# Performance work log

Measured on AMD Instinct MI355X. Metric: run time of the kernel, lower is better.

Reference implementation:

```python
import jax, jax.numpy as jnp
import numpy as np

N = 20000        # number of protein atoms
C_IN = 32        # input atom features
C = 128          # hidden_channels
E_BOND = 80000   # directed bond edges (~2 bonds/atom, both directions)
R = 4.0          # radius_graph radius (Angstrom)
BOX = 55.0       # box side -> ~32 neighbors within r=4


def _radius_graph_np(pos, r):
    # symmetric radius graph, no self loops (PyG radius_graph, neighbor cap omitted)
    r2 = r * r
    rows, cols = [], []
    for i0 in range(0, pos.shape[0], 500):
        chunk = pos[i0:i0 + 500]
        d2 = ((chunk[:, None, :] - pos[None, :, :]) ** 2).sum(-1)
        m = d2 < r2
        m[np.arange(chunk.shape[0]), i0 + np.arange(chunk.shape[0])] = False
        ii, jj = np.nonzero(m)
        rows.append(jj)            # source j
        cols.append(ii + i0)       # target i
    return np.stack([np.concatenate(rows), np.concatenate(cols)]).astype(np.int32)


def setup_inputs() -> dict:
    key = jax.random.key(0)
    ks = jax.random.split(key, 12)
    rng = np.random.default_rng(0)

    pos = rng.uniform(0.0, BOX, (N, 3)).astype(np.float32)
    r_edge_index = jnp.asarray(_radius_graph_np(pos, R))

    half = E_BOND // 2
    s = rng.integers(0, N, half); d = rng.integers(0, N, half)
    edge_index = jnp.asarray(np.stack([np.concatenate([s, d]), np.concatenate([d, s])]).astype(np.int32))

    def lin(k, fin, fout):
        lim = 1.0 / np.sqrt(fin)
        kw, kb = jax.random.split(k)
        W = jax.random.uniform(kw, (fin, fout), jnp.float32, -lim, lim)
        b = jax.random.uniform(kb, (fout,), jnp.float32, -lim, lim)
        return W, b

    We1, be1 = lin(ks[0], C_IN, C)
    We2, be2 = lin(ks[1], C, C)
    Wf1, bf1 = lin(ks[2], 2 * C, C); Ws1, bs1 = lin(ks[3], 2 * C, C)
    Wf2, bf2 = lin(ks[4], 2 * C, C); Ws2, bs2 = lin(ks[5], 2 * C, C)
    Wf3, bf3 = lin(ks[6], 2 * C, C); Ws3, bs3 = lin(ks[7], 2 * C, C)
    Wf4, bf4 = lin(ks[8], 2 * C, C); Ws4, bs4 = lin(ks[9], 2 * C, C)

    x_prot = jax.random.normal(ks[10], (N, C_IN), jnp.float32)
    v_prot = jnp.asarray(pos)

    return dict(x_prot=x_prot, v_prot=v_prot, edge_index=edge_index, r_edge_index=r_edge_index,
                We1=We1, be1=be1, We2=We2, be2=be2,
                Wf1=Wf1, bf1=bf1, Ws1=Ws1, bs1=bs1,
                Wf2=Wf2, bf2=bf2, Ws2=Ws2, bs2=bs2,
                Wf3=Wf3, bf3=bf3, Ws3=Ws3, bs3=bs3,
                Wf4=Wf4, bf4=bf4, Ws4=Ws4, bs4=bs4)


def _cgconv(x, ei, Wf, bf, Ws, bs):
    # PyG CGConv: z = [x_i, x_j]; out = x + mean_j sigmoid(lin_f(z)) * softplus(lin_s(z))
    src, dst = ei[0], ei[1]              # source j -> target i
    z = jnp.concatenate([x[dst], x[src]], axis=1)          # [E, 2C]
    msg = jax.nn.sigmoid(z @ Wf + bf) * jax.nn.softplus(z @ Ws + bs)  # [E, C]
    agg = jax.ops.segment_sum(msg, dst, num_segments=x.shape[0])
    cnt = jax.ops.segment_sum(jnp.ones((ei.shape[1],), x.dtype), dst, num_segments=x.shape[0])
    return x + agg / jnp.maximum(cnt, 1.0)[:, None]


def reference(x_prot, v_prot, edge_index, r_edge_index,
              We1, be1, We2, be2,
              Wf1, bf1, Ws1, bs1, Wf2, bf2, Ws2, bs2,
              Wf3, bf3, Ws3, bs3, Wf4, bf4, Ws4, bs4):
    # embed MLP (PyG MLP with batch-norm at init == identity): Linear->ReLU->Linear
    x = jax.nn.relu(x_prot @ We1 + be1) @ We2 + be2
    # bond convs
    x = jax.nn.relu(_cgconv(x, edge_index, Wf1, bf1, Ws1, bs1))
    x = jax.nn.relu(_cgconv(x, edge_index, Wf2, bf2, Ws2, bs2))
    # radius convs (r_edge_index = radius_graph(v_prot, r=4), precomputed in setup)
    x = jax.nn.relu(_cgconv(x, r_edge_index, Wf3, bf3, Ws3, bs3))
    x = jax.nn.relu(_cgconv(x, r_edge_index, Wf4, bf4, Ws4, bs4))
    return jax.nn.relu(x)  # final self.act (idempotent on ReLU output)
```

## Files before the change

kernel.cpp:

```cpp
#include <hip/hip_runtime.h>
#include <hip/hip_bf16.h>

#define NN 20000
#define CC 128

typedef __attribute__((ext_vector_type(8))) _Float16 half8;
typedef __attribute__((ext_vector_type(2))) _Float16 half2v;
typedef __attribute__((ext_vector_type(4))) float f32x4;

typedef const __attribute__((address_space(1))) void gv_t;
typedef __attribute__((address_space(3))) void sv_t;

__global__ __launch_bounds__(256) void conv_all_kernel(
    const float* __restrict__ Wf0, const float* __restrict__ Ws0,
    const float* __restrict__ Wf1, const float* __restrict__ Ws1,
    const float* __restrict__ Wf2, const float* __restrict__ Ws2,
    const float* __restrict__ Wf3, const float* __restrict__ Ws3,
    const float* __restrict__ We2, const float* __restrict__ We1,
    const float* __restrict__ xprot,
    _Float16* __restrict__ WctAll, _Float16* __restrict__ Wcte,
    _Float16* __restrict__ Wt1, _Float16* __restrict__ xp16) {
    int id = blockIdx.x * 256 + threadIdx.x;
    if (id < 262144) {
        int Lw = id >> 16;
        int i = id & 65535;
        int c = i & 511;
        int k = i >> 9;
        const float* Wfp = (Lw == 0) ? Wf0 : (Lw == 1) ? Wf1 : (Lw == 2) ? Wf2 : Wf3;
        const float* Wsp = (Lw == 0) ? Ws0 : (Lw == 1) ? Ws1 : (Lw == 2) ? Ws2 : Ws3;
        float v;
        if (c < 128) v = Wfp[k * 128 + c];
        else if (c < 256) v = Wfp[(128 + k) * 128 + (c - 128)];
        else if (c < 384) v = Wsp[k * 128 + (c - 256)];
        else v = Wsp[(128 + k) * 128 + (c - 384)];
        WctAll[Lw * 65536 + c * 128 + k] = (_Float16)v;
    } else if (id < 278528) {
        int i = id - 262144;
        int c = i & 127;
        int k = i >> 7;
        Wcte[c * 128 + k] = (_Float16)We2[k * 128 + c];
    } else if (id < 282624) {
        int i = id - 278528;
        int c = i & 127;
        int k = i >> 7;
        Wt1[c * 32 + k] = (_Float16)We1[k * 128 + c];
    } else {
        int i = id - 282624;
        xp16[i] = (_Float16)xprot[i];
    }
}

__global__ __launch_bounds__(256) void enc1_mfma_kernel(
    const _Float16* __restrict__ A, const _Float16* __restrict__ Wt1,
    const float* __restrict__ b, _Float16* __restrict__ Y) {
    int t = threadIdx.x;
    int wid = t >> 6, l = t & 63;
    int lr = l & 15, hi = l >> 4;
    int m0 = blockIdx.x * 128 + wid * 32;
    half8 af[2];
#pragma unroll
    for (int m = 0; m < 2; ++m) {
        int row = m0 + m * 16 + lr;
        half8 v = {0, 0, 0, 0, 0, 0, 0, 0};
        if (row < NN) v = *(const half8*)(A + (long)row * 32 + hi * 8);
        af[m] = v;
    }
    f32x4 acc[2][8] = {};
#pragma unroll
    for (int n = 0; n < 8; ++n) {
        int col = n * 16 + lr;
        half8 bg = *(const half8*)(Wt1 + (long)col * 32 + hi * 8);
#pragma unroll
        for (int m = 0; m < 2; ++m)
            acc[m][n] = __builtin_amdgcn_mfma_f32_16x16x32_f16(af[m], bg, acc[m][n], 0, 0, 0);
    }
#pragma unroll
    for (int n = 0; n < 8; ++n) {
        int col = n * 16 + lr;
        float bb = b[col];
#pragma unroll
        for (int m = 0; m < 2; ++m) {
#pragma unroll
            for (int q = 0; q < 4; ++q) {
                int row = m0 + m * 16 + hi * 4 + q;
                if (row < NN)
                    Y[(long)row * 128 + col] = (_Float16)fmaxf(acc[m][n][q] + bb, 0.0f);
            }
        }
    }
}

__global__ __launch_bounds__(256) void gemm_mfma_kernel(
    const _Float16* __restrict__ A, const _Float16* __restrict__ Wt,
    const float* __restrict__ bias0, const float* __restrict__ bias1,
    _Float16* __restrict__ outH, float* __restrict__ outF,
    _Float16* __restrict__ outF16, int M, int mode) {
    __shared__ _Float16 lds[32768];
    int t = threadIdx.x;
    int w = t >> 6, l = t & 63;
    int m0 = blockIdx.x * 128;
    int n0 = blockIdx.y * 128;
    {
        int rin = l >> 4;
        int cs = l & 15;
#pragma unroll
        for (int j = 0; j < 8; ++j) {
            int r = w * 32 + j * 4 + rin;
            int g = cs ^ (r & 7);
            int grow = m0 + r;
            if (grow > M - 1) grow = M - 1;
            const _Float16* srcA = A + (long)grow * 128 + g * 8;
            __builtin_amdgcn_global_load_lds((gv_t*)srcA,
                (sv_t*)&lds[(w * 32 + j * 4) * 128], 16, 0, 0);
            const _Float16* srcB = Wt + (long)(n0 + r) * 128 + g * 8;
            __builtin_amdgcn_global_load_lds((gv_t*)srcB,
                (sv_t*)&lds[16384 + (w * 32 + j * 4) * 128], 16, 0, 0);
        }
    }
    __syncthreads();
    int wm = w >> 1, wn = w & 1;
    int lr = l & 15, hi = l >> 4;
    f32x4 acc[4][4] = {};
#pragma unroll
    for (int ks = 0; ks < 4; ++ks) {
        int cidx = 4 * ks + hi;
        half8 af[4], bg[4];
#pragma unroll
        for (int m = 0; m < 4; ++m) {
            int row = wm * 64 + m * 16 + lr;
            af[m] = *(const half8*)(&lds[row * 128 + (cidx ^ (row & 7)) * 8]);
        }
#pragma unroll
        for (int n = 0; n < 4; ++n) {
            int row = wn * 64 + n * 16 + lr;
            bg[n] = *(const half8*)(&lds[16384 + row * 128 + (cidx ^ (row & 7)) * 8]);
        }
#pragma unroll
        for (int m = 0; m < 4; ++m)
#pragma unroll
            for (int n = 0; n < 4; ++n)
                acc[m][n] = __builtin_amdgcn_mfma_f32_16x16x32_f16(
                    af[m], bg[n], acc[m][n], 0, 0, 0);
    }
    if (mode == 0) {
        __syncthreads();
        const float S = 1.44269504f;
#pragma unroll
        for (int n = 0; n < 4; ++n) {
            int cl = wn * 64 + n * 16 + lr;
            int gcol = n0 + cl;
            float badd = (gcol < 128) ? bias0[gcol]
                       : ((gcol >= 256 && gcol < 384) ? bias1[gcol - 256] : 0.0f);
#pragma unroll
            for (int m = 0; m < 4; ++m)
#pragma unroll
                for (int q = 0; q < 4; ++q) {
                    int rl = wm * 64 + m * 16 + hi * 4 + q;
                    lds[rl * 144 + cl] = (_Float16)((acc[m][n][q] + badd) * S);
                }
        }
        __syncthreads();
#pragma unroll
        for (int i = 0; i < 8; ++i) {
            int id = t + 256 * i;
            int row = id >> 4, ch = id & 15;
            int grow = m0 + row;
            if (grow < M) {
                half8 v = *(const half8*)(&lds[row * 144 + ch * 8]);
                *(half8*)(&outH[(long)grow * 512 + n0 + ch * 8]) = v;
            }
        }
    } else {
#pragma unroll
        for (int n = 0; n < 4; ++n) {
            int gcol = n0 + wn * 64 + n * 16 + lr;
            float badd = bias0[gcol];
#pragma unroll
            for (int m = 0; m < 4; ++m)
#pragma unroll
                for (int q = 0; q < 4; ++q) {
                    int grow = m0 + wm * 64 + m * 16 + hi * 4 + q;
                    if (grow < M) {
                        float v = acc[m][n][q] + badd;
                        outF[(long)grow * 128 + gcol] = v;
                        outF16[(long)grow * 128 + gcol] = (_Float16)v;
                    }
                }
        }
    }
}

__global__ __launch_bounds__(256) void count_int_kernel(
    const int* __restrict__ dst, int E, int* __restrict__ cnt) {
    int e = blockIdx.x * 256 + threadIdx.x;
    if (e < E) atomicAdd(&cnt[dst[e]], 1);
}

__global__ __launch_bounds__(1024) void scan_kernel(
    const int* __restrict__ cnt, int* __restrict__ off) {
    __shared__ int part[1024];
    int t = threadIdx.x;
    int base = t * 20;
    int loc[20];
    int s = 0;
#pragma unroll
    for (int i = 0; i < 20; ++i) {
        int idx = base + i;
        int v = (idx < NN) ? cnt[idx] : 0;
        loc[i] = s;
        s += v;
    }
    part[t] = s;
    __syncthreads();
    for (int d = 1; d < 1024; d <<= 1) {
        int v = (t >= d) ? part[t - d] : 0;
        __syncthreads();
        part[t] += v;
        __syncthreads();
    }
    int pre = (t > 0) ? part[t - 1] : 0;
#pragma unroll
    for (int i = 0; i < 20; ++i) {
        int idx = base + i;
        if (idx < NN) off[idx] = pre + loc[i];
    }
    if (t == 1023) off[NN] = part[1023];
}

__global__ __launch_bounds__(256) void scatter_kernel(
    const int* __restrict__ src, const int* __restrict__ dst, int E,
    const int* __restrict__ off, int* __restrict__ cur, int* __restrict__ eid) {
    int e = blockIdx.x * 256 + threadIdx.x;
    if (e < E) {
        int d = dst[e];
        int p = off[d] + atomicAdd(&cur[d], 1);
        eid[p] = src[e];
    }
}

__global__ __launch_bounds__(256) void csr_off_kernel(
    const int* __restrict__ dst, int E, int N1, int* __restrict__ off) {
    int n = blockIdx.x * 256 + threadIdx.x;
    if (n >= N1) return;
    int lo = 0, hi = E;
    while (lo < hi) {
        int mid = (lo + hi) >> 1;
        if (dst[mid] < n) lo = mid + 1;
        else hi = mid;
    }
    off[n] = lo;
}

__global__ __launch_bounds__(256) void node_agg_kernel(
    const _Float16* __restrict__ H, const int* __restrict__ srcArr,
    const int* __restrict__ off, const float* __restrict__ xin,
    float* __restrict__ xout, _Float16* __restrict__ xh, int write_h) {
    int n = blockIdx.x * 4 + (threadIdx.x >> 6);
    int nu = __builtin_amdgcn_readfirstlane(n);
    int l = threadIdx.x & 63;
    const half2v* H2 = (const half2v*)H;
    const half2v* hrow = H2 + (long)nu * 256;
    half2v fdh = hrow[l];
    half2v sdh = hrow[128 + l];
    int e0 = __builtin_amdgcn_readfirstlane(off[nu]);
    int e1 = __builtin_amdgcn_readfirstlane(off[nu + 1]);
    float ax = 0.0f, ay = 0.0f;
#define EDGEC(fv, sv)                                                        \
    {                                                                        \
        half2v fsum = fdh + (fv);                                            \
        half2v ssum = sdh + (sv);                                            \
        float fx = (float)fsum.x, fy = (float)fsum.y;                        \
        float sx = (float)ssum.x, sy = (float)ssum.y;                        \
        float rx = __builtin_amdgcn_rcpf(1.0f + __builtin_amdgcn_exp2f(-fx)); \
        float ry = __builtin_amdgcn_rcpf(1.0f + __builtin_amdgcn_exp2f(-fy)); \
        float spx = fmaxf(sx, 0.0f) +                                        \
                    __builtin_amdgcn_logf(1.0f + __builtin_amdgcn_exp2f(-fabsf(sx))); \
        float spy = fmaxf(sy, 0.0f) +                                        \
                    __builtin_amdgcn_logf(1.0f + __builtin_amdgcn_exp2f(-fabsf(sy))); \
        ax += rx * spx;                                                      \
        ay += ry * spy;                                                      \
    }
    int e = e0;
    for (; e + 3 < e1; e += 4) {
        int s0 = srcArr[e], s1 = srcArr[e + 1];
        int s2 = srcArr[e + 2], s3 = srcArr[e + 3];
        const half2v* h0 = H2 + (long)s0 * 256;
        const half2v* h1 = H2 + (long)s1 * 256;
        const half2v* h2 = H2 + (long)s2 * 256;
        const half2v* h3 = H2 + (long)s3 * 256;
        half2v f0 = h0[64 + l], g0 = h0[192 + l];
        half2v f1 = h1[64 + l], g1 = h1[192 + l];
        half2v f2 = h2[64 + l], g2 = h2[192 + l];
        half2v f3 = h3[64 + l], g3 = h3[192 + l];
        EDGEC(f0, g0) EDGEC(f1, g1) EDGEC(f2, g2) EDGEC(f3, g3)
    }
    for (; e < e1; ++e) {
        int s0 = srcArr[e];
        const half2v* h0 = H2 + (long)s0 * 256;
        half2v f0 = h0[64 + l], g0 = h0[192 + l];
        EDGEC(f0, g0)
    }
#undef EDGEC
    float inv = 0.6931471805599453f *
                __builtin_amdgcn_rcpf(fmaxf((float)(e1 - e0), 1.0f));
    float2 xv = ((const float2*)xin)[(long)nu * 64 + l];
    float ox = fmaxf(xv.x + ax * inv, 0.0f);
    float oy = fmaxf(xv.y + ay * inv, 0.0f);
    ((float2*)xout)[(long)nu * 64 + l] = make_float2(ox, oy);
    if (write_h) {
        half2v oh;
        oh.x = (_Float16)ox;
        oh.y = (_Float16)oy;
        ((half2v*)xh)[(long)nu * 64 + l] = oh;
    }
}

extern "C" void kernel_launch(void* const* d_in, const int* in_sizes, int n_in,
                              void* d_out, int out_size, void* d_ws, size_t ws_size,
                              hipStream_t stream) {
    const float* x_prot = (const float*)d_in[0];
    const int* eb = (const int*)d_in[2];
    const int* er = (const int*)d_in[3];
    int Eb = in_sizes[2] / 2;
    int Er = in_sizes[3] / 2;
    const float* We1 = (const float*)d_in[4];
    const float* be1 = (const float*)d_in[5];
    const float* We2 = (const float*)d_in[6];
    const float* be2 = (const float*)d_in[7];
    const float* Wf[4]  = {(const float*)d_in[8],  (const float*)d_in[12],
                           (const float*)d_in[16], (const float*)d_in[20]};
    const float* bf[4]  = {(const float*)d_in[9],  (const float*)d_in[13],
                           (const float*)d_in[17], (const float*)d_in[21]};
    const float* Wsp[4] = {(const float*)d_in[10], (const float*)d_in[14],
                           (const float*)d_in[18], (const float*)d_in[22]};
    const float* bsp[4] = {(const float*)d_in[11], (const float*)d_in[15],
                           (const float*)d_in[19], (const float*)d_in[23]};

    char* ws = (char*)d_ws;
    float*     xbuf  = (float*)ws;
    _Float16*  xhf   = (_Float16*)(ws + 10240000);
    _Float16*  H     = (_Float16*)(ws + 15360000);
    _Float16*  xp16  = (_Float16*)(ws + 35840000);
    int*       cntI  = (int*)(ws + 37120000);
    int*       curB  = (int*)(ws + 37200000);
    int*       offB  = (int*)(ws + 37280000);
    int*       offR  = (int*)(ws + 37360016);
    int*       eidB  = (int*)(ws + 37440032);
    _Float16*  WctAll= (_Float16*)(ws + 37760032);
    _Float16*  Wcte  = (_Float16*)(ws + 38284320);
    _Float16*  Wt1   = (_Float16*)(ws + 38317088);

    const int* srcB = eb;
    const int* dstB = eb + Eb;
    const int* srcR = er;

    conv_all_kernel<<<3604, 256, 0, stream>>>(
        Wf[0], Wsp[0], Wf[1], Wsp[1], Wf[2], Wsp[2], Wf[3], Wsp[3],
        We2, We1, x_prot, WctAll, Wcte, Wt1, xp16);

    hipMemsetAsync(cntI, 0, 160000, stream);
    count_int_kernel<<<(Eb + 255) / 256, 256, 0, stream>>>(dstB, Eb, cntI);
    scan_kernel<<<1, 1024, 0, stream>>>(cntI, offB);
    scatter_kernel<<<(Eb + 255) / 256, 256, 0, stream>>>(srcB, dstB, Eb, offB, curB, eidB);
    csr_off_kernel<<<(NN + 256) / 256, 256, 0, stream>>>(er + Er, Er, NN + 1, offR);

    enc1_mfma_kernel<<<157, 256, 0, stream>>>(xp16, Wt1, be1, H);
    {
        dim3 g(157, 1);
        gemm_mfma_kernel<<<g, 256, 0, stream>>>(H, Wcte, be2, be2, nullptr,
                                                xbuf, xhf, NN, 1);
    }

    for (int L = 0; L < 4; ++L) {
        dim3 g(157, 4);
        gemm_mfma_kernel<<<g, 256, 0, stream>>>(xhf, WctAll + L * 65536, bf[L],
                                                bsp[L], H, nullptr, nullptr, NN, 0);
        const int* sArr = (L < 2) ? eidB : srcR;
        const int* oArr = (L < 2) ? offB : offR;
        float* xout = (L == 3) ? (float*)d_out : xbuf;
        node_agg_kernel<<<NN / 4, 256, 0, stream>>>(H, sArr, oArr, xbuf, xout,
                                                    xhf, (L == 3) ? 0 : 1);
    }
    (void)n_in; (void)out_size; (void)ws_size;
}
```

Before: 230.4 us.

## Replace sigmoid/softplus transcendentals with LDS lookup tables in node aggregation

Precomputes a 2048-entry sigmoid table and a 1024-entry softplus-correction table (in log2 domain) on the GPU, loads them into shared memory per block, and replaces per-edge exp/rcp/log calls with clamped table lookups. The aggregation kernel also becomes a grid-stride loop over nodes with 2048 blocks, which amortizes the table load across many nodes. This trades transcendental ALU work for LDS reads and adds quantization error from nearest-bin lookup over a clamped range.

Result: slower. 239.4 us (+3.9%).

```diff
diff --git a/kernel.cpp b/kernel.cpp
--- a/kernel.cpp
+++ b/kernel.cpp
@@ -10,6 +10,8 @@
 
 typedef const __attribute__((address_space(1))) void gv_t;
 typedef __attribute__((address_space(3))) void sv_t;
+
+#define TBL_SCALE 85.333336f
 
 __global__ __launch_bounds__(256) void conv_all_kernel(
     const float* __restrict__ Wf0, const float* __restrict__ Ws0,
@@ -19,7 +21,8 @@
     const float* __restrict__ We2, const float* __restrict__ We1,
     const float* __restrict__ xprot,
     _Float16* __restrict__ WctAll, _Float16* __restrict__ Wcte,
-    _Float16* __restrict__ Wt1, _Float16* __restrict__ xp16) {
+    _Float16* __restrict__ Wt1, _Float16* __restrict__ xp16,
+    float* __restrict__ tbl) {
     int id = blockIdx.x * 256 + threadIdx.x;
     if (id < 262144) {
         int Lw = id >> 16;
@@ -44,9 +47,17 @@
         int c = i & 127;
         int k = i >> 7;
         Wt1[c * 32 + k] = (_Float16)We1[k * 128 + c];
-    } else {
+    } else if (id < 922624) {
         int i = id - 282624;
         xp16[i] = (_Float16)xprot[i];
+    } else if (id < 924672) {
+        int i = id - 922624;
+        float fp = (i + 0.5f) * (24.0f / 2048.0f) - 12.0f;
+        tbl[i] = 1.0f / (1.0f + exp2f(-fp));
+    } else if (id < 925696) {
+        int j = id - 924672;
+        float tt = (j + 0.5f) * (12.0f / 1024.0f);
+        tbl[2048 + j] = log2f(1.0f + exp2f(-tt));
     }
 }
 
@@ -254,64 +265,78 @@
 __global__ __launch_bounds__(256) void node_agg_kernel(
     const _Float16* __restrict__ H, const int* __restrict__ srcArr,
     const int* __restrict__ off, const float* __restrict__ xin,
-    float* __restrict__ xout, _Float16* __restrict__ xh, int write_h) {
-    int n = blockIdx.x * 4 + (threadIdx.x >> 6);
-    int nu = __builtin_amdgcn_readfirstlane(n);
-    int l = threadIdx.x & 63;
+    float* __restrict__ xout, _Float16* __restrict__ xh,
+    const float* __restrict__ tblG, int write_h) {
+    __shared__ float sigT[2048];
+    __shared__ float cT[1024];
+    int t = threadIdx.x;
+    for (int i = t; i < 3072; i += 256) {
+        float v = tblG[i];
+        if (i < 2048) sigT[i] = v;
+        else cT[i - 2048] = v;
+    }
+    __syncthreads();
+    int l = t & 63;
+    int wn = t >> 6;
     const half2v* H2 = (const half2v*)H;
-    const half2v* hrow = H2 + (long)nu * 256;
-    half2v fdh = hrow[l];
-    half2v sdh = hrow[128 + l];
-    int e0 = __builtin_amdgcn_readfirstlane(off[nu]);
-    int e1 = __builtin_amdgcn_readfirstlane(off[nu + 1]);
-    float ax = 0.0f, ay = 0.0f;
-#define EDGEC(fv, sv)                                                        \
-    {                                                                        \
-        half2v fsum = fdh + (fv);                                            \
-        half2v ssum = sdh + (sv);                                            \
-        float fx = (float)fsum.x, fy = (float)fsum.y;                        \
-        float sx = (float)ssum.x, sy = (float)ssum.y;                        \
-        float rx = __builtin_amdgcn_rcpf(1.0f + __builtin_amdgcn_exp2f(-fx)); \
-        float ry = __builtin_amdgcn_rcpf(1.0f + __builtin_amdgcn_exp2f(-fy)); \
-        float spx = fmaxf(sx, 0.0f) +                                        \
-                    __builtin_amdgcn_logf(1.0f + __builtin_amdgcn_exp2f(-fabsf(sx))); \
-        float spy = fmaxf(sy, 0.0f) +                                        \
-                    __builtin_amdgcn_logf(1.0f + __builtin_amdgcn_exp2f(-fabsf(sy))); \
-        ax += rx * spx;                                                      \
-        ay += ry * spy;                                                      \
-    }
-    int e = e0;
-    for (; e + 3 < e1; e += 4) {
-        int s0 = srcArr[e], s1 = srcArr[e + 1];
-        int s2 = srcArr[e + 2], s3 = srcArr[e + 3];
-        const half2v* h0 = H2 + (long)s0 * 256;
-        const half2v* h1 = H2 + (long)s1 * 256;
-        const half2v* h2 = H2 + (long)s2 * 256;
-        const half2v* h3 = H2 + (long)s3 * 256;
-        half2v f0 = h0[64 + l], g0 = h0[192 + l];
-        half2v f1 = h1[64 + l], g1 = h1[192 + l];
-        half2v f2 = h2[64 + l], g2 = h2[192 + l];
-        half2v f3 = h3[64 + l], g3 = h3[192 + l];
-        EDGEC(f0, g0) EDGEC(f1, g1) EDGEC(f2, g2) EDGEC(f3, g3)
-    }
-    for (; e < e1; ++e) {
-        int s0 = srcArr[e];
-        const half2v* h0 = H2 + (long)s0 * 256;
-        half2v f0 = h0[64 + l], g0 = h0[192 + l];
-        EDGEC(f0, g0)
-    }
+    for (int n = blockIdx.x * 4 + wn; n < NN; n += gridDim.x * 4) {
+        int nu = __builtin_amdgcn_readfirstlane(n);
+        const half2v* hrow = H2 + (long)nu * 256;
+        half2v fdh = hrow[l];
+        half2v sdh = hrow[128 + l];
+        int e0 = __builtin_amdgcn_readfirstlane(off[nu]);
+        int e1 = __builtin_amdgcn_readfirstlane(off[nu + 1]);
+        float ax = 0.0f, ay = 0.0f;
+#define EDGEC(fv, sv)                                                      \
+    {                                                                      \
+        half2v fsum = fdh + (fv);                                          \
+        half2v ssum = sdh + (sv);                                          \
+        float fx = (float)fsum.x, fy = (float)fsum.y;                      \
+        float sx = (float)ssum.x, sy = (float)ssum.y;                      \
+        float tfx = fminf(fmaxf(__builtin_fmaf(fx, TBL_SCALE, 1024.0f), 0.0f), 2047.0f); \
+        float tfy = fminf(fmaxf(__builtin_fmaf(fy, TBL_SCALE, 1024.0f), 0.0f), 2047.0f); \
+        float tsx = fminf(fabsf(sx) * TBL_SCALE, 1023.0f);                 \
+        float tsy = fminf(fabsf(sy) * TBL_SCALE, 1023.0f);                 \
+        float gx = sigT[(int)tfx];                                         \
+        float gy = sigT[(int)tfy];                                         \
+        float spx = fmaxf(sx, 0.0f) + cT[(int)tsx];                        \
+        float spy = fmaxf(sy, 0.0f) + cT[(int)tsy];                        \
+        ax += gx * spx;                                                    \
+        ay += gy * spy;                                                    \
+    }
+        int e = e0;
+        for (; e + 3 < e1; e += 4) {
+            int s0 = srcArr[e], s1 = srcArr[e + 1];
+            int s2 = srcArr[e + 2], s3 = srcArr[e + 3];
+            const half2v* h0 = H2 + (long)s0 * 256;
+            const half2v* h1 = H2 + (long)s1 * 256;
+            const half2v* h2 = H2 + (long)s2 * 256;
+            const half2v* h3 = H2 + (long)s3 * 256;
+            half2v f0 = h0[64 + l], g0 = h0[192 + l];
+            half2v f1 = h1[64 + l], g1 = h1[192 + l];
+            half2v f2 = h2[64 + l], g2 = h2[192 + l];
+            half2v f3 = h3[64 + l], g3 = h3[192 + l];
+            EDGEC(f0, g0) EDGEC(f1, g1) EDGEC(f2, g2) EDGEC(f3, g3)
+        }
+        for (; e < e1; ++e) {
+            int s0 = srcArr[e];
+            const half2v* h0 = H2 + (long)s0 * 256;
+            half2v f0 = h0[64 + l], g0 = h0[192 + l];
+            EDGEC(f0, g0)
+        }
 #undef EDGEC
-    float inv = 0.6931471805599453f *
-                __builtin_amdgcn_rcpf(fmaxf((float)(e1 - e0), 1.0f));
-    float2 xv = ((const float2*)xin)[(long)nu * 64 + l];
-    float ox = fmaxf(xv.x + ax * inv, 0.0f);
-    float oy = fmaxf(xv.y + ay * inv, 0.0f);
-    ((float2*)xout)[(long)nu * 64 + l] = make_float2(ox, oy);
-    if (write_h) {
-        half2v oh;
-        oh.x = (_Float16)ox;
-        oh.y = (_Float16)oy;
-        ((half2v*)xh)[(long)nu * 64 + l] = oh;
+        float inv = 0.6931471805599453f *
+                    __builtin_amdgcn_rcpf(fmaxf((float)(e1 - e0), 1.0f));
+        float2 xv = ((const float2*)xin)[(long)nu * 64 + l];
+        float ox = fmaxf(xv.x + ax * inv, 0.0f);
+        float oy = fmaxf(xv.y + ay * inv, 0.0f);
+        ((float2*)xout)[(long)nu * 64 + l] = make_float2(ox, oy);
+        if (write_h) {
+            half2v oh;
+            oh.x = (_Float16)ox;
+            oh.y = (_Float16)oy;
+            ((half2v*)xh)[(long)nu * 64 + l] = oh;
+        }
     }
 }
 
@@ -349,14 +374,15 @@
     _Float16*  WctAll= (_Float16*)(ws + 37760032);
     _Float16*  Wcte  = (_Float16*)(ws + 38284320);
     _Float16*  Wt1   = (_Float16*)(ws + 38317088);
+    float*     tbl   = (float*)(ws + 38325280);
 
     const int* srcB = eb;
     const int* dstB = eb + Eb;
     const int* srcR = er;
 
-    conv_all_kernel<<<3604, 256, 0, stream>>>(
+    conv_all_kernel<<<3616, 256, 0, stream>>>(
         Wf[0], Wsp[0], Wf[1], Wsp[1], Wf[2], Wsp[2], Wf[3], Wsp[3],
-        We2, We1, x_prot, WctAll, Wcte, Wt1, xp16);
+        We2, We1, x_prot, WctAll, Wcte, Wt1, xp16, tbl);
 
     hipMemsetAsync(cntI, 0, 160000, stream);
     count_int_kernel<<<(Eb + 255) / 256, 256, 0, stream>>>(dstB, Eb, cntI);
@@ -378,8 +404,8 @@
         const int* sArr = (L < 2) ? eidB : srcR;
         const int* oArr = (L < 2) ? offB : offR;
         float* xout = (L == 3) ? (float*)d_out : xbuf;
-        node_agg_kernel<<<NN / 4, 256, 0, stream>>>(H, sArr, oArr, xbuf, xout,
-                                                    xhf, (L == 3) ? 0 : 1);
+        node_agg_kernel<<<2048, 256, 0, stream>>>(H, sArr, oArr, xbuf, xout,
+                                                  xhf, tbl, (L == 3) ? 0 : 1);
     }
     (void)n_in; (void)out_size; (void)ws_size;
 }
```

## Store source-side gate projections in FP8 and interleave per-node H layout

Applied to the files above, without the earlier changes.

The projection output H is repacked so each node's destination-side FP16 filter and softplus values sit interleaved, followed by FP8-quantized source-side values packed as filter/softplus pairs. The aggregation kernel then gathers only 4 bytes per lane per neighbor instead of two 4-byte FP16 loads from separate regions. This cuts gather traffic across the roughly 640K radius edges. In exchange, source-side precision drops to FP8, which risks accuracy, and the GEMM epilogue now issues narrower scattered stores.

After: 258.7 us. +12.3%, slower.

```diff
diff --git a/kernel.cpp b/kernel.cpp
--- a/kernel.cpp
+++ b/kernel.cpp
@@ -5,8 +5,10 @@
 #define CC 128
 
 typedef __attribute__((ext_vector_type(8))) _Float16 half8;
+typedef __attribute__((ext_vector_type(4))) _Float16 half4;
 typedef __attribute__((ext_vector_type(2))) _Float16 half2v;
 typedef __attribute__((ext_vector_type(4))) float f32x4;
+typedef __attribute__((ext_vector_type(2))) float f32x2;
 
 typedef const __attribute__((address_space(1))) void gv_t;
 typedef __attribute__((address_space(3))) void sv_t;
@@ -93,7 +95,7 @@
 __global__ __launch_bounds__(256) void gemm_mfma_kernel(
     const _Float16* __restrict__ A, const _Float16* __restrict__ Wt,
     const float* __restrict__ bias0, const float* __restrict__ bias1,
-    _Float16* __restrict__ outH, float* __restrict__ outF,
+    char* __restrict__ outH, float* __restrict__ outF,
     _Float16* __restrict__ outF16, int M, int mode) {
     __shared__ _Float16 lds[32768];
     int t = threadIdx.x;
@@ -161,13 +163,24 @@
         }
         __syncthreads();
 #pragma unroll
-        for (int i = 0; i < 8; ++i) {
-            int id = t + 256 * i;
-            int row = id >> 4, ch = id & 15;
+        for (int k = 0; k < 32; ++k) {
+            int id = t + 256 * k;
+            int i = id & 63, row = id >> 6;
             int grow = m0 + row;
-            if (grow < M) {
-                half8 v = *(const half8*)(&lds[row * 144 + ch * 8]);
-                *(half8*)(&outH[(long)grow * 512 + n0 + ch * 8]) = v;
+            if (grow >= M) continue;
+            uint hv = *(const uint*)(&lds[row * 144 + 2 * i]);
+            char* Hb = outH + (long)grow * 1024;
+            if (n0 == 0) {
+                *(uint*)(Hb + i * 8) = hv;
+            } else if (n0 == 256) {
+                *(uint*)(Hb + i * 8 + 4) = hv;
+            } else {
+                half2v hp = *(const half2v*)(&hv);
+                int p = __builtin_amdgcn_cvt_pk_fp8_f32(
+                    (float)hp.x, (float)hp.y, 0, false);
+                short pv = (short)(p & 0xffff);
+                if (n0 == 128) *(short*)(Hb + 512 + i * 4) = pv;
+                else           *(short*)(Hb + 512 + i * 4 + 2) = pv;
             }
         }
     } else {
@@ -252,53 +265,47 @@
 }
 
 __global__ __launch_bounds__(256) void node_agg_kernel(
-    const _Float16* __restrict__ H, const int* __restrict__ srcArr,
+    const char* __restrict__ H, const int* __restrict__ srcArr,
     const int* __restrict__ off, const float* __restrict__ xin,
     float* __restrict__ xout, _Float16* __restrict__ xh, int write_h) {
     int n = blockIdx.x * 4 + (threadIdx.x >> 6);
     int nu = __builtin_amdgcn_readfirstlane(n);
     int l = threadIdx.x & 63;
-    const half2v* H2 = (const half2v*)H;
-    const half2v* hrow = H2 + (long)nu * 256;
-    half2v fdh = hrow[l];
-    half2v sdh = hrow[128 + l];
+    half4 d4 = *(const half4*)(H + (long)nu * 1024 + l * 8);
+    float fdx = (float)d4[0], fdy = (float)d4[1];
+    float sdx = (float)d4[2], sdy = (float)d4[3];
     int e0 = __builtin_amdgcn_readfirstlane(off[nu]);
     int e1 = __builtin_amdgcn_readfirstlane(off[nu + 1]);
     float ax = 0.0f, ay = 0.0f;
-#define EDGEC(fv, sv)                                                        \
-    {                                                                        \
-        half2v fsum = fdh + (fv);                                            \
-        half2v ssum = sdh + (sv);                                            \
-        float fx = (float)fsum.x, fy = (float)fsum.y;                        \
-        float sx = (float)ssum.x, sy = (float)ssum.y;                        \
+#define EDGEC(wv)                                                             \
+    {                                                                         \
+        f32x2 fsp = __builtin_amdgcn_cvt_pk_f32_fp8((int)(wv), false);        \
+        f32x2 ssp = __builtin_amdgcn_cvt_pk_f32_fp8((int)(wv), true);         \
+        float fx = fdx + fsp[0], fy = fdy + fsp[1];                           \
+        float sx = sdx + ssp[0], sy = sdy + ssp[1];                           \
         float rx = __builtin_amdgcn_rcpf(1.0f + __builtin_amdgcn_exp2f(-fx)); \
         float ry = __builtin_amdgcn_rcpf(1.0f + __builtin_amdgcn_exp2f(-fy)); \
-        float spx = fmaxf(sx, 0.0f) +                                        \
+        float spx = fmaxf(sx, 0.0f) +                                         \
                     __builtin_amdgcn_logf(1.0f + __builtin_amdgcn_exp2f(-fabsf(sx))); \
-        float spy = fmaxf(sy, 0.0f) +                                        \
+        float spy = fmaxf(sy, 0.0f) +                                         \
                     __builtin_amdgcn_logf(1.0f + __builtin_amdgcn_exp2f(-fabsf(sy))); \
-        ax += rx * spx;                                                      \
-        ay += ry * spy;                                                      \
+        ax += rx * spx;                                                       \
+        ay += ry * spy;                                                       \
     }
     int e = e0;
     for (; e + 3 < e1; e += 4) {
         int s0 = srcArr[e], s1 = srcArr[e + 1];
         int s2 = srcArr[e + 2], s3 = srcArr[e + 3];
-        const half2v* h0 = H2 + (long)s0 * 256;
-        const half2v* h1 = H2 + (long)s1 * 256;
-        const half2v* h2 = H2 + (long)s2 * 256;
-        const half2v* h3 = H2 + (long)s3 * 256;
-        half2v f0 = h0[64 + l], g0 = h0[192 + l];
-        half2v f1 = h1[64 + l], g1 = h1[192 + l];
-        half2v f2 = h2[64 + l], g2 = h2[192 + l];
-        half2v f3 = h3[64 + l], g3 = h3[192 + l];
-        EDGEC(f0, g0) EDGEC(f1, g1) EDGEC(f2, g2) EDGEC(f3, g3)
+        uint w0 = *(const uint*)(H + (long)s0 * 1024 + 512 + l * 4);
+        uint w1 = *(const uint*)(H + (long)s1 * 1024 + 512 + l * 4);
+        uint w2 = *(const uint*)(H + (long)s2 * 1024 + 512 + l * 4);
+        uint w3 = *(const uint*)(H + (long)s3 * 1024 + 512 + l * 4);
+        EDGEC(w0) EDGEC(w1) EDGEC(w2) EDGEC(w3)
     }
     for (; e < e1; ++e) {
         int s0 = srcArr[e];
-        const half2v* h0 = H2 + (long)s0 * 256;
-        half2v f0 = h0[64 + l], g0 = h0[192 + l];
-        EDGEC(f0, g0)
+        uint w0 = *(const uint*)(H + (long)s0 * 1024 + 512 + l * 4);
+        EDGEC(w0)
     }
 #undef EDGEC
     float inv = 0.6931471805599453f *
@@ -339,7 +346,7 @@
     char* ws = (char*)d_ws;
     float*     xbuf  = (float*)ws;
     _Float16*  xhf   = (_Float16*)(ws + 10240000);
-    _Float16*  H     = (_Float16*)(ws + 15360000);
+    char*      H     = (char*)(ws + 15360000);
     _Float16*  xp16  = (_Float16*)(ws + 35840000);
     int*       cntI  = (int*)(ws + 37120000);
     int*       curB  = (int*)(ws + 37200000);
@@ -364,11 +371,11 @@
     scatter_kernel<<<(Eb + 255) / 256, 256, 0, stream>>>(srcB, dstB, Eb, offB, curB, eidB);
     csr_off_kernel<<<(NN + 256) / 256, 256, 0, stream>>>(er + Er, Er, NN + 1, offR);
 
-    enc1_mfma_kernel<<<157, 256, 0, stream>>>(xp16, Wt1, be1, H);
+    enc1_mfma_kernel<<<157, 256, 0, stream>>>(xp16, Wt1, be1, (_Float16*)H);
     {
         dim3 g(157, 1);
-        gemm_mfma_kernel<<<g, 256, 0, stream>>>(H, Wcte, be2, be2, nullptr,
-                                                xbuf, xhf, NN, 1);
+        gemm_mfma_kernel<<<g, 256, 0, stream>>>((_Float16*)H, Wcte, be2, be2,
+                                                nullptr, xbuf, xhf, NN, 1);
     }
 
     for (int L = 0; L < 4; ++L) {
```
